# Performance work log

Measured on AMD Instinct MI355X. Metric: run time of the kernel, lower is better.

The kernel has to match this reference:

```python
import jax, jax.numpy as jnp
import numpy as np

EPS_DISC = 1e-9  # matches mamba_discretization denominator epsilon


def setup_inputs() -> dict:
    key = jax.random.key(0)
    ks = jax.random.split(key, 12)
    L, D, N, W = 2048, 1024, 16, 3
    s = 0.02  # small init scale to keep softplus/exp well-behaved
    u_seq = jax.random.normal(ks[0], (L, D), jnp.float32)
    # A_log = log(-A) with A = randn*0.1 - 1.0  -> log of a value near 1
    A_log = jnp.log(jnp.clip(1.0 - 0.1 * jax.random.normal(ks[1], (N,), jnp.float32), 0.5, 1.5))
    dt_w = jax.random.normal(ks[2], (D, D), jnp.float32) * s
    dt_b = jax.random.normal(ks[3], (D,), jnp.float32) * s
    B_w = jax.random.normal(ks[4], (N, D), jnp.float32) * s
    B_b = jax.random.normal(ks[5], (N,), jnp.float32) * s
    C_w = jax.random.normal(ks[6], (N, D), jnp.float32) * s
    C_b = jax.random.normal(ks[7], (N,), jnp.float32) * s
    D_w = jnp.ones((D,), jnp.float32)
    scale = jnp.ones((), jnp.float32)
    init_w = jax.random.normal(ks[8], (D * N, D * W), jnp.float32) * s
    init_b = jax.random.normal(ks[9], (D * N,), jnp.float32) * s
    return {"u_seq": u_seq, "A_log": A_log, "dt_w": dt_w, "dt_b": dt_b,
            "B_w": B_w, "B_b": B_b, "C_w": C_w, "C_b": C_b,
            "D_w": D_w, "scale": scale, "init_w": init_w, "init_b": init_b}


def reference(u_seq, A_log, dt_w, dt_b, B_w, B_b, C_w, C_b, D_w, scale, init_w, init_b):
    L, D = u_seq.shape
    N = A_log.shape[0]
    init_window = init_w.shape[1] // D
    # Initial state h0 = init_estimator(u[:W].flatten()).view(D, N)
    u_prefix = u_seq[:init_window].reshape(-1)
    h0 = (u_prefix @ init_w.T + init_b).reshape(D, N)
    # Input-dependent SSM parameters (all L timesteps at once)
    dt = jax.nn.softplus(u_seq @ dt_w.T + dt_b)           # [L, D]
    B = u_seq @ B_w.T + B_b                               # [L, N]
    C = u_seq @ C_w.T + C_b                               # [L, N]
    A = -jnp.exp(A_log)                                   # [N]
    dtA = dt[:, :, None] * A                              # [L, D, N]
    dA = jnp.exp(dtA)                                     # [L, D, N]
    dB = jnp.expm1(dtA) / (dtA + EPS_DISC) * B[:, None, :]  # ZOH discretization
    Bu = dB * u_seq[:, :, None]                           # [L, D, N]

    # Sequential selective-scan recurrence: h_t = dA_t * h_{t-1} + Bu_t
    def step(h, inp):
        dA_t, Bu_t = inp
        h = dA_t * h + Bu_t
        return h, h

    _, h_hist = jax.lax.scan(step, h0, (dA, Bu))          # [L, D, N]
    y_raw = jnp.einsum('ln,ldn->ld', C, h_hist) + D_w * u_seq
    return jax.nn.softplus(y_raw) * jnp.maximum(scale, 0.5)
```

## Files before the change

### kernel.cpp

```cpp
#include <hip/hip_runtime.h>
#include <hip/hip_bf16.h>

typedef __attribute__((ext_vector_type(8))) short short8v;
typedef __attribute__((ext_vector_type(4))) float f32x4;

#define L_SEQ 2048
#define D_DIM 1024
#define N_DIM 16
#define T_CHUNK 32
#define NCHUNK (L_SEQ / T_CHUNK)
#define EPS_DISC 1e-9f

__device__ __forceinline__ float softplusf(float x) {
    return (x > 15.f) ? x : __logf(1.f + __expf(x));
}

__device__ __forceinline__ unsigned short f2bf(float f) {
    unsigned int u = __float_as_uint(f);
    u += 0x7FFFu + ((u >> 16) & 1u);
    return (unsigned short)(u >> 16);
}
__device__ __forceinline__ unsigned int pack2(float a, float b) {
    return (unsigned int)f2bf(a) | ((unsigned int)f2bf(b) << 16);
}

__global__ __launch_bounds__(256) void fm_params(const float* __restrict__ u,
                                                 const float* __restrict__ dt_w,
                                                 const float* __restrict__ dt_b,
                                                 const float* __restrict__ B_w,
                                                 const float* __restrict__ B_b,
                                                 const float* __restrict__ C_w,
                                                 const float* __restrict__ C_b,
                                                 const float* __restrict__ init_w,
                                                 const float* __restrict__ init_b,
                                                 float* __restrict__ dt_out,
                                                 float* __restrict__ Bout,
                                                 float* __restrict__ Cout,
                                                 float* __restrict__ h0) {
    __shared__ unsigned int As[128 * 16];
    __shared__ unsigned int Bs[128 * 16];
    const int b = blockIdx.x;
    const int t = threadIdx.x;

    if (b < 128) {
        const int bm   = b & 15;
        const int bn   = b >> 4;
        const int row  = t >> 1;
        const int half = t & 1;
        const int swz  = (row >> 1) & 3;
        const int lane = t & 63;
        const int wid  = t >> 6;
        const int wm   = wid >> 1, wn = wid & 1;
        const int lrow = lane & 15, lq = lane >> 4;

        const float* uptr = u + (bm * 128 + row) * 1024 + half * 16;
        const float* wptr = dt_w + (bn * 128 + row) * 1024 + half * 16;

        f32x4 acc[4][4];
#pragma unroll
        for (int mi = 0; mi < 4; ++mi)
#pragma unroll
            for (int ni = 0; ni < 4; ++ni) acc[mi][ni] = (f32x4){0.f, 0.f, 0.f, 0.f};

        for (int k0 = 0; k0 < 1024; k0 += 32) {
            __syncthreads();
            {
                const float4* p = (const float4*)(uptr + k0);
                float4 a0 = p[0], a1 = p[1], a2 = p[2], a3 = p[3];
                uint4 c0 = make_uint4(pack2(a0.x, a0.y), pack2(a0.z, a0.w),
                                      pack2(a1.x, a1.y), pack2(a1.z, a1.w));
                uint4 c1 = make_uint4(pack2(a2.x, a2.y), pack2(a2.z, a2.w),
                                      pack2(a3.x, a3.y), pack2(a3.z, a3.w));
                const int kb0 = (half * 2) ^ swz, kb1 = (half * 2 + 1) ^ swz;
                *(uint4*)&As[row * 16 + kb0 * 4] = c0;
                *(uint4*)&As[row * 16 + kb1 * 4] = c1;

                const float4* q = (const float4*)(wptr + k0);
                float4 b0 = q[0], b1 = q[1], b2 = q[2], b3 = q[3];
                uint4 d0 = make_uint4(pack2(b0.x, b0.y), pack2(b0.z, b0.w),
                                      pack2(b1.x, b1.y), pack2(b1.z, b1.w));
                uint4 d1 = make_uint4(pack2(b2.x, b2.y), pack2(b2.z, b2.w),
                                      pack2(b3.x, b3.y), pack2(b3.z, b3.w));
                *(uint4*)&Bs[row * 16 + kb0 * 4] = d0;
                *(uint4*)&Bs[row * 16 + kb1 * 4] = d1;
            }
            __syncthreads();
            short8v af[4], bf[4];
#pragma unroll
            for (int mi = 0; mi < 4; ++mi) {
                const int ar = wm * 64 + mi * 16 + lrow;
                const int kb = lq ^ ((ar >> 1) & 3);
                af[mi] = *(const short8v*)&As[ar * 16 + kb * 4];
            }
#pragma unroll
            for (int ni = 0; ni < 4; ++ni) {
                const int br = wn * 64 + ni * 16 + lrow;
                const int kb = lq ^ ((br >> 1) & 3);
                bf[ni] = *(const short8v*)&Bs[br * 16 + kb * 4];
            }
#pragma unroll
            for (int mi = 0; mi < 4; ++mi)
#pragma unroll
                for (int ni = 0; ni < 4; ++ni)
                    acc[mi][ni] = __builtin_amdgcn_mfma_f32_16x16x32_bf16(af[mi], bf[ni], acc[mi][ni], 0, 0, 0);
        }

#pragma unroll
        for (int mi = 0; mi < 4; ++mi)
#pragma unroll
            for (int ni = 0; ni < 4; ++ni) {
                const int cg = bn * 128 + wn * 64 + ni * 16 + lrow;
                const float bv = dt_b[cg];
#pragma unroll
                for (int j = 0; j < 4; ++j) {
                    const int rg = bm * 128 + wm * 64 + mi * 16 + lq * 4 + j;
                    dt_out[rg * 1024 + cg] = softplusf(acc[mi][ni][j] + bv);
                }
            }
    } else if (b < 384) {
        const int tid = (b - 128) * 256 + t;
        const int l = tid >> 5;
        const int col = tid & 31;
        const float* wrow = (col < 16) ? (B_w + col * 1024) : (C_w + (col - 16) * 1024);
        const float4* w4 = (const float4*)wrow;
        const float4* u4 = (const float4*)(u + l * 1024);
        float acc = 0.f;
#pragma unroll 8
        for (int j = 0; j < 256; ++j) {
            float4 a = u4[j], bb = w4[j];
            acc += a.x * bb.x + a.y * bb.y + a.z * bb.z + a.w * bb.w;
        }
        if (col < 16) Bout[l * 16 + col] = acc + B_b[col];
        else          Cout[l * 16 + (col - 16)] = acc + C_b[col - 16];
    } else {
        const int lane = t & 63;
        const int row  = (b - 384) * 4 + (t >> 6);
        const float4* w4 = (const float4*)(init_w + row * 3072);
        const float4* u4 = (const float4*)u;
        float acc = 0.f;
#pragma unroll
        for (int s = 0; s < 12; ++s) {
            float4 a = w4[s * 64 + lane];
            float4 bb = u4[s * 64 + lane];
            acc += a.x * bb.x + a.y * bb.y + a.z * bb.z + a.w * bb.w;
        }
#pragma unroll
        for (int off = 32; off > 0; off >>= 1) acc += __shfl_down(acc, off);
        if (lane == 0) h0[row] = acc + init_b[row];
    }
}

__global__ __launch_bounds__(256) void fm_scan_phase1(const float* __restrict__ dt,
                                                      const float* __restrict__ Bm,
                                                      const float* __restrict__ u,
                                                      const float* __restrict__ A_log,
                                                      float* __restrict__ ap,
                                                      float* __restrict__ hl) {
    const int t = threadIdx.x;
    const int c = blockIdx.x >> 2;
    const int d = ((blockIdx.x & 3) << 8) | t;
    float An[16];
#pragma unroll
    for (int n = 0; n < 16; ++n) An[n] = -__expf(A_log[n]);
    float h[16], p[16];
#pragma unroll
    for (int n = 0; n < 16; ++n) { h[n] = 0.f; p[n] = 1.f; }

    const int l0 = c * T_CHUNK;
    for (int i = 0; i < T_CHUNK; ++i) {
        const int l = l0 + i;
        const float dtld = dt[l * D_DIM + d];
        const float uld  = u[l * D_DIM + d];
        const float4 b0 = *(const float4*)&Bm[l * 16 + 0];
        const float4 b1 = *(const float4*)&Bm[l * 16 + 4];
        const float4 b2 = *(const float4*)&Bm[l * 16 + 8];
        const float4 b3 = *(const float4*)&Bm[l * 16 + 12];
        auto body = [&](int n, float bn) {
            const float x = dtld * An[n];
            const float e = __expf(x);
            const float coef = (e - 1.f) * __builtin_amdgcn_rcpf(x + EPS_DISC);
            const float bu = coef * bn * uld;
            p[n] *= e;
            h[n] = fmaf(e, h[n], bu);
        };
        body(0, b0.x);  body(1, b0.y);  body(2, b0.z);  body(3, b0.w);
        body(4, b1.x);  body(5, b1.y);  body(6, b1.z);  body(7, b1.w);
        body(8, b2.x);  body(9, b2.y);  body(10, b2.z); body(11, b2.w);
        body(12, b3.x); body(13, b3.y); body(14, b3.z); body(15, b3.w);
    }
    const int base = c * (D_DIM * N_DIM) + d * 16;
    *(float4*)&ap[base + 0]  = make_float4(p[0], p[1], p[2], p[3]);
    *(float4*)&ap[base + 4]  = make_float4(p[4], p[5], p[6], p[7]);
    *(float4*)&ap[base + 8]  = make_float4(p[8], p[9], p[10], p[11]);
    *(float4*)&ap[base + 12] = make_float4(p[12], p[13], p[14], p[15]);
    *(float4*)&hl[base + 0]  = make_float4(h[0], h[1], h[2], h[3]);
    *(float4*)&hl[base + 4]  = make_float4(h[4], h[5], h[6], h[7]);
    *(float4*)&hl[base + 8]  = make_float4(h[8], h[9], h[10], h[11]);
    *(float4*)&hl[base + 12] = make_float4(h[12], h[13], h[14], h[15]);
}

__global__ __launch_bounds__(64) void fm_scan_phase2(const float* __restrict__ h0,
                                                     float* __restrict__ ap,
                                                     const float* __restrict__ hl) {
    const int tid = blockIdx.x * 64 + threadIdx.x;
    float h = h0[tid];
#pragma unroll 8
    for (int c = 0; c < NCHUNK; ++c) {
        const int idx = c * (D_DIM * N_DIM) + tid;
        const float a = ap[idx];
        const float b = hl[idx];
        ap[idx] = h;
        h = fmaf(a, h, b);
    }
}

__global__ __launch_bounds__(256) void fm_scan_phase3(const float* __restrict__ dt,
                                                      const float* __restrict__ Bm,
                                                      const float* __restrict__ Cm,
                                                      const float* __restrict__ u,
                                                      const float* __restrict__ A_log,
                                                      const float* __restrict__ hstart,
                                                      const float* __restrict__ D_w,
                                                      const float* __restrict__ scale,
                                                      float* __restrict__ out) {
    const int t = threadIdx.x;
    const int c = blockIdx.x >> 2;
    const int d = ((blockIdx.x & 3) << 8) | t;
    float An[16];
#pragma unroll
    for (int n = 0; n < 16; ++n) An[n] = -__expf(A_log[n]);
    float h[16];
    const int base = c * (D_DIM * N_DIM) + d * 16;
    {
        float4 h0v = *(const float4*)&hstart[base + 0];
        float4 h1v = *(const float4*)&hstart[base + 4];
        float4 h2v = *(const float4*)&hstart[base + 8];
        float4 h3v = *(const float4*)&hstart[base + 12];
        h[0] = h0v.x; h[1] = h0v.y; h[2] = h0v.z; h[3] = h0v.w;
        h[4] = h1v.x; h[5] = h1v.y; h[6] = h1v.z; h[7] = h1v.w;
        h[8] = h2v.x; h[9] = h2v.y; h[10] = h2v.z; h[11] = h2v.w;
        h[12] = h3v.x; h[13] = h3v.y; h[14] = h3v.z; h[15] = h3v.w;
    }
    const float scl = fmaxf(scale[0], 0.5f);
    const float dw = D_w[d];
    const int l0 = c * T_CHUNK;
    for (int i = 0; i < T_CHUNK; ++i) {
        const int l = l0 + i;
        const float dtld = dt[l * D_DIM + d];
        const float uld  = u[l * D_DIM + d];
        const float4 b0 = *(const float4*)&Bm[l * 16 + 0];
        const float4 b1 = *(const float4*)&Bm[l * 16 + 4];
        const float4 b2 = *(const float4*)&Bm[l * 16 + 8];
        const float4 b3 = *(const float4*)&Bm[l * 16 + 12];
        const float4 c0 = *(const float4*)&Cm[l * 16 + 0];
        const float4 c1 = *(const float4*)&Cm[l * 16 + 4];
        const float4 c2 = *(const float4*)&Cm[l * 16 + 8];
        const float4 c3 = *(const float4*)&Cm[l * 16 + 12];
        float y = 0.f;
        auto body = [&](int n, float bn, float cn) {
            const float x = dtld * An[n];
            const float e = __expf(x);
            const float coef = (e - 1.f) * __builtin_amdgcn_rcpf(x + EPS_DISC);
            const float bu = coef * bn * uld;
            h[n] = fmaf(e, h[n], bu);
            y = fmaf(cn, h[n], y);
        };
        body(0, b0.x, c0.x);   body(1, b0.y, c0.y);   body(2, b0.z, c0.z);   body(3, b0.w, c0.w);
        body(4, b1.x, c1.x);   body(5, b1.y, c1.y);   body(6, b1.z, c1.z);   body(7, b1.w, c1.w);
        body(8, b2.x, c2.x);   body(9, b2.y, c2.y);   body(10, b2.z, c2.z);  body(11, b2.w, c2.w);
        body(12, b3.x, c3.x);  body(13, b3.y, c3.y);  body(14, b3.z, c3.z);  body(15, b3.w, c3.w);
        y = fmaf(dw, uld, y);
        out[l * D_DIM + d] = softplusf(y) * scl;
    }
}

extern "C" void kernel_launch(void* const* d_in, const int* in_sizes, int n_in,
                              void* d_out, int out_size, void* d_ws, size_t ws_size,
                              hipStream_t stream) {
    const float* u      = (const float*)d_in[0];
    const float* A_log  = (const float*)d_in[1];
    const float* dt_w   = (const float*)d_in[2];
    const float* dt_b   = (const float*)d_in[3];
    const float* B_w    = (const float*)d_in[4];
    const float* B_b    = (const float*)d_in[5];
    const float* C_w    = (const float*)d_in[6];
    const float* C_b    = (const float*)d_in[7];
    const float* D_w    = (const float*)d_in[8];
    const float* scale  = (const float*)d_in[9];
    const float* init_w = (const float*)d_in[10];
    const float* init_b = (const float*)d_in[11];
    float* out = (float*)d_out;

    float* ws = (float*)d_ws;
    float* dt = ws;
    float* Bm = dt + 2097152;
    float* Cm = Bm + 32768;
    float* h0 = Cm + 32768;
    float* ap = h0 + 16384;
    float* hl = ap + 1048576;

    hipLaunchKernelGGL(fm_params, dim3(4480), dim3(256), 0, stream,
                       u, dt_w, dt_b, B_w, B_b, C_w, C_b, init_w, init_b,
                       dt, Bm, Cm, h0);
    hipLaunchKernelGGL(fm_scan_phase1, dim3(256), dim3(256), 0, stream, dt, Bm, u, A_log, ap, hl);
    hipLaunchKernelGGL(fm_scan_phase2, dim3(256), dim3(64), 0, stream, h0, ap, hl);
    hipLaunchKernelGGL(fm_scan_phase3, dim3(256), dim3(256), 0, stream, dt, Bm, Cm, u, A_log, ap, D_w, scale, out);
}
```

Before: 120.3 us.

## Fuse all phases into one cooperative persistent kernel with grid syncs

Merges the parameter GEMM, the chunk scan, the cross-chunk carry and the output pass into a single cooperative kernel that loops over tiles and separates phases with grid.sync. It also splits each channel's 16 states across two threads, doubling the thread count in the scan phases and combining the partial outputs with a shuffle. The aim is to remove launch gaps and tail effects between the four kernels and to use more of the GPU in the scan phases. In exchange, the GEMM phase now runs as a persistent loop with a grid limited by occupancy, plus the cost of the grid barriers, and the old four-kernel path is kept as a fallback.

```diff
diff --git a/kernel.cpp b/kernel.cpp
--- a/kernel.cpp
+++ b/kernel.cpp
@@ -1,5 +1,8 @@
 #include <hip/hip_runtime.h>
 #include <hip/hip_bf16.h>
+#include <hip/hip_cooperative_groups.h>
+
+namespace cg = cooperative_groups;
 
 typedef __attribute__((ext_vector_type(8))) short short8v;
 typedef __attribute__((ext_vector_type(4))) float f32x4;
@@ -24,27 +27,18 @@
     return (unsigned int)f2bf(a) | ((unsigned int)f2bf(b) << 16);
 }
 
-__global__ __launch_bounds__(256) void fm_params(const float* __restrict__ u,
-                                                 const float* __restrict__ dt_w,
-                                                 const float* __restrict__ dt_b,
-                                                 const float* __restrict__ B_w,
-                                                 const float* __restrict__ B_b,
-                                                 const float* __restrict__ C_w,
-                                                 const float* __restrict__ C_b,
-                                                 const float* __restrict__ init_w,
-                                                 const float* __restrict__ init_b,
-                                                 float* __restrict__ dt_out,
-                                                 float* __restrict__ Bout,
-                                                 float* __restrict__ Cout,
-                                                 float* __restrict__ h0) {
-    __shared__ unsigned int As[128 * 16];
-    __shared__ unsigned int Bs[128 * 16];
-    const int b = blockIdx.x;
+__device__ void phaseA_tile(int tile, unsigned int* As, unsigned int* Bs,
+                            const float* __restrict__ u,
+                            const float* __restrict__ dt_w, const float* __restrict__ dt_b,
+                            const float* __restrict__ B_w, const float* __restrict__ B_b,
+                            const float* __restrict__ C_w, const float* __restrict__ C_b,
+                            const float* __restrict__ init_w, const float* __restrict__ init_b,
+                            float* __restrict__ dt, float* __restrict__ Bm,
+                            float* __restrict__ Cm, float* __restrict__ h0) {
     const int t = threadIdx.x;
-
-    if (b < 128) {
-        const int bm   = b & 15;
-        const int bn   = b >> 4;
+    if (tile < 128) {
+        const int bm   = tile & 15;
+        const int bn   = tile >> 4;
         const int row  = t >> 1;
         const int half = t & 1;
         const int swz  = (row >> 1) & 3;
@@ -109,16 +103,17 @@
         for (int mi = 0; mi < 4; ++mi)
 #pragma unroll
             for (int ni = 0; ni < 4; ++ni) {
-                const int cg = bn * 128 + wn * 64 + ni * 16 + lrow;
-                const float bv = dt_b[cg];
+                const int cg_ = bn * 128 + wn * 64 + ni * 16 + lrow;
+                const float bv = dt_b[cg_];
 #pragma unroll
                 for (int j = 0; j < 4; ++j) {
                     const int rg = bm * 128 + wm * 64 + mi * 16 + lq * 4 + j;
-                    dt_out[rg * 1024 + cg] = softplusf(acc[mi][ni][j] + bv);
+                    dt[rg * 1024 + cg_] = softplusf(acc[mi][ni][j] + bv);
                 }
             }
-    } else if (b < 384) {
-        const int tid = (b - 128) * 256 + t;
+        __syncthreads();
+    } else if (tile < 384) {
+        const int tid = (tile - 128) * 256 + t;
         const int l = tid >> 5;
         const int col = tid & 31;
         const float* wrow = (col < 16) ? (B_w + col * 1024) : (C_w + (col - 16) * 1024);
@@ -130,11 +125,11 @@
             float4 a = u4[j], bb = w4[j];
             acc += a.x * bb.x + a.y * bb.y + a.z * bb.z + a.w * bb.w;
         }
-        if (col < 16) Bout[l * 16 + col] = acc + B_b[col];
-        else          Cout[l * 16 + (col - 16)] = acc + C_b[col - 16];
+        if (col < 16) Bm[l * 16 + col] = acc + B_b[col];
+        else          Cm[l * 16 + (col - 16)] = acc + C_b[col - 16];
     } else {
         const int lane = t & 63;
-        const int row  = (b - 384) * 4 + (t >> 6);
+        const int row  = (tile - 384) * 4 + (t >> 6);
         const float4* w4 = (const float4*)(init_w + row * 3072);
         const float4* u4 = (const float4*)u;
         float acc = 0.f;
@@ -150,31 +145,30 @@
     }
 }
 
-__global__ __launch_bounds__(256) void fm_scan_phase1(const float* __restrict__ dt,
-                                                      const float* __restrict__ Bm,
-                                                      const float* __restrict__ u,
-                                                      const float* __restrict__ A_log,
-                                                      float* __restrict__ ap,
-                                                      float* __restrict__ hl) {
-    const int t = threadIdx.x;
-    const int c = blockIdx.x >> 2;
-    const int d = ((blockIdx.x & 3) << 8) | t;
-    float An[16];
-#pragma unroll
-    for (int n = 0; n < 16; ++n) An[n] = -__expf(A_log[n]);
-    float h[16], p[16];
-#pragma unroll
-    for (int n = 0; n < 16; ++n) { h[n] = 0.f; p[n] = 1.f; }
+__device__ void phaseB_tile(int tile,
+                            const float* __restrict__ dt, const float* __restrict__ Bm,
+                            const float* __restrict__ u, const float* __restrict__ A_log,
+                            float* __restrict__ ap, float* __restrict__ hl) {
+    const int t    = threadIdx.x;
+    const int c    = tile >> 3;
+    const int dblk = tile & 7;
+    const int dd   = t >> 1;
+    const int nh   = t & 1;
+    const int d    = dblk * 128 + dd;
+    float An[8];
+#pragma unroll
+    for (int n = 0; n < 8; ++n) An[n] = -__expf(A_log[nh * 8 + n]);
+    float h[8], p[8];
+#pragma unroll
+    for (int n = 0; n < 8; ++n) { h[n] = 0.f; p[n] = 1.f; }
 
     const int l0 = c * T_CHUNK;
     for (int i = 0; i < T_CHUNK; ++i) {
         const int l = l0 + i;
         const float dtld = dt[l * D_DIM + d];
         const float uld  = u[l * D_DIM + d];
-        const float4 b0 = *(const float4*)&Bm[l * 16 + 0];
-        const float4 b1 = *(const float4*)&Bm[l * 16 + 4];
-        const float4 b2 = *(const float4*)&Bm[l * 16 + 8];
-        const float4 b3 = *(const float4*)&Bm[l * 16 + 12];
+        const float4 b0 = *(const float4*)&Bm[l * 16 + nh * 8];
+        const float4 b1 = *(const float4*)&Bm[l * 16 + nh * 8 + 4];
         auto body = [&](int n, float bn) {
             const float x = dtld * An[n];
             const float e = __expf(x);
@@ -183,63 +177,56 @@
             p[n] *= e;
             h[n] = fmaf(e, h[n], bu);
         };
-        body(0, b0.x);  body(1, b0.y);  body(2, b0.z);  body(3, b0.w);
-        body(4, b1.x);  body(5, b1.y);  body(6, b1.z);  body(7, b1.w);
-        body(8, b2.x);  body(9, b2.y);  body(10, b2.z); body(11, b2.w);
-        body(12, b3.x); body(13, b3.y); body(14, b3.z); body(15, b3.w);
-    }
-    const int base = c * (D_DIM * N_DIM) + d * 16;
-    *(float4*)&ap[base + 0]  = make_float4(p[0], p[1], p[2], p[3]);
-    *(float4*)&ap[base + 4]  = make_float4(p[4], p[5], p[6], p[7]);
-    *(float4*)&ap[base + 8]  = make_float4(p[8], p[9], p[10], p[11]);
-    *(float4*)&ap[base + 12] = make_float4(p[12], p[13], p[14], p[15]);
-    *(float4*)&hl[base + 0]  = make_float4(h[0], h[1], h[2], h[3]);
-    *(float4*)&hl[base + 4]  = make_float4(h[4], h[5], h[6], h[7]);
-    *(float4*)&hl[base + 8]  = make_float4(h[8], h[9], h[10], h[11]);
-    *(float4*)&hl[base + 12] = make_float4(h[12], h[13], h[14], h[15]);
-}
-
-__global__ __launch_bounds__(64) void fm_scan_phase2(const float* __restrict__ h0,
-                                                     float* __restrict__ ap,
-                                                     const float* __restrict__ hl) {
-    const int tid = blockIdx.x * 64 + threadIdx.x;
-    float h = h0[tid];
+        body(0, b0.x); body(1, b0.y); body(2, b0.z); body(3, b0.w);
+        body(4, b1.x); body(5, b1.y); body(6, b1.z); body(7, b1.w);
+    }
+    const int base = c * (D_DIM * N_DIM) + d * 16 + nh * 8;
+    *(float4*)&ap[base + 0] = make_float4(p[0], p[1], p[2], p[3]);
+    *(float4*)&ap[base + 4] = make_float4(p[4], p[5], p[6], p[7]);
+    *(float4*)&hl[base + 0] = make_float4(h[0], h[1], h[2], h[3]);
+    *(float4*)&hl[base + 4] = make_float4(h[4], h[5], h[6], h[7]);
+}
+
+__device__ void phaseC_group(int g,
+                             const float* __restrict__ h0,
+                             float* __restrict__ ap, const float* __restrict__ hl) {
+    const int t = threadIdx.x;
+    if (t < 64) {
+        const int ch = g * 64 + t;
+        float h = h0[ch];
 #pragma unroll 8
-    for (int c = 0; c < NCHUNK; ++c) {
-        const int idx = c * (D_DIM * N_DIM) + tid;
-        const float a = ap[idx];
-        const float b = hl[idx];
-        ap[idx] = h;
-        h = fmaf(a, h, b);
-    }
-}
-
-__global__ __launch_bounds__(256) void fm_scan_phase3(const float* __restrict__ dt,
-                                                      const float* __restrict__ Bm,
-                                                      const float* __restrict__ Cm,
-                                                      const float* __restrict__ u,
-                                                      const float* __restrict__ A_log,
-                                                      const float* __restrict__ hstart,
-                                                      const float* __restrict__ D_w,
-                                                      const float* __restrict__ scale,
-                                                      float* __restrict__ out) {
-    const int t = threadIdx.x;
-    const int c = blockIdx.x >> 2;
-    const int d = ((blockIdx.x & 3) << 8) | t;
-    float An[16];
-#pragma unroll
-    for (int n = 0; n < 16; ++n) An[n] = -__expf(A_log[n]);
-    float h[16];
-    const int base = c * (D_DIM * N_DIM) + d * 16;
+        for (int c = 0; c < NCHUNK; ++c) {
+            const int idx = c * (D_DIM * N_DIM) + ch;
+            const float a = ap[idx];
+            const float b = hl[idx];
+            ap[idx] = h;
+            h = fmaf(a, h, b);
+        }
+    }
+}
+
+__device__ void phaseD_tile(int tile,
+                            const float* __restrict__ dt, const float* __restrict__ Bm,
+                            const float* __restrict__ Cm, const float* __restrict__ u,
+                            const float* __restrict__ A_log, const float* __restrict__ hstart,
+                            const float* __restrict__ D_w, const float* __restrict__ scale,
+                            float* __restrict__ out) {
+    const int t    = threadIdx.x;
+    const int c    = tile >> 3;
+    const int dblk = tile & 7;
+    const int dd   = t >> 1;
+    const int nh   = t & 1;
+    const int d    = dblk * 128 + dd;
+    float An[8];
+#pragma unroll
+    for (int n = 0; n < 8; ++n) An[n] = -__expf(A_log[nh * 8 + n]);
+    float h[8];
+    const int base = c * (D_DIM * N_DIM) + d * 16 + nh * 8;
     {
         float4 h0v = *(const float4*)&hstart[base + 0];
         float4 h1v = *(const float4*)&hstart[base + 4];
-        float4 h2v = *(const float4*)&hstart[base + 8];
-        float4 h3v = *(const float4*)&hstart[base + 12];
         h[0] = h0v.x; h[1] = h0v.y; h[2] = h0v.z; h[3] = h0v.w;
         h[4] = h1v.x; h[5] = h1v.y; h[6] = h1v.z; h[7] = h1v.w;
-        h[8] = h2v.x; h[9] = h2v.y; h[10] = h2v.z; h[11] = h2v.w;
-        h[12] = h3v.x; h[13] = h3v.y; h[14] = h3v.z; h[15] = h3v.w;
     }
     const float scl = fmaxf(scale[0], 0.5f);
     const float dw = D_w[d];
@@ -248,14 +235,10 @@
         const int l = l0 + i;
         const float dtld = dt[l * D_DIM + d];
         const float uld  = u[l * D_DIM + d];
-        const float4 b0 = *(const float4*)&Bm[l * 16 + 0];
-        const float4 b1 = *(const float4*)&Bm[l * 16 + 4];
-        const float4 b2 = *(const float4*)&Bm[l * 16 + 8];
-        const float4 b3 = *(const float4*)&Bm[l * 16 + 12];
-        const float4 c0 = *(const float4*)&Cm[l * 16 + 0];
-        const float4 c1 = *(const float4*)&Cm[l * 16 + 4];
-        const float4 c2 = *(const float4*)&Cm[l * 16 + 8];
-        const float4 c3 = *(const float4*)&Cm[l * 16 + 12];
+        const float4 b0 = *(const float4*)&Bm[l * 16 + nh * 8];
+        const float4 b1 = *(const float4*)&Bm[l * 16 + nh * 8 + 4];
+        const float4 c0 = *(const float4*)&Cm[l * 16 + nh * 8];
+        const float4 c1 = *(const float4*)&Cm[l * 16 + nh * 8 + 4];
         float y = 0.f;
         auto body = [&](int n, float bn, float cn) {
             const float x = dtld * An[n];
@@ -265,13 +248,91 @@
             h[n] = fmaf(e, h[n], bu);
             y = fmaf(cn, h[n], y);
         };
-        body(0, b0.x, c0.x);   body(1, b0.y, c0.y);   body(2, b0.z, c0.z);   body(3, b0.w, c0.w);
-        body(4, b1.x, c1.x);   body(5, b1.y, c1.y);   body(6, b1.z, c1.z);   body(7, b1.w, c1.w);
-        body(8, b2.x, c2.x);   body(9, b2.y, c2.y);   body(10, b2.z, c2.z);  body(11, b2.w, c2.w);
-        body(12, b3.x, c3.x);  body(13, b3.y, c3.y);  body(14, b3.z, c3.z);  body(15, b3.w, c3.w);
-        y = fmaf(dw, uld, y);
-        out[l * D_DIM + d] = softplusf(y) * scl;
-    }
+        body(0, b0.x, c0.x); body(1, b0.y, c0.y); body(2, b0.z, c0.z); body(3, b0.w, c0.w);
+        body(4, b1.x, c1.x); body(5, b1.y, c1.y); body(6, b1.z, c1.z); body(7, b1.w, c1.w);
+        y += __shfl_xor(y, 1);
+        if (nh == 0) {
+            const float yv = fmaf(dw, uld, y);
+            out[l * D_DIM + d] = softplusf(yv) * scl;
+        }
+    }
+}
+
+__global__ __launch_bounds__(256, 2) void fm_mega(const float* __restrict__ u,
+                                                  const float* __restrict__ A_log,
+                                                  const float* __restrict__ dt_w,
+                                                  const float* __restrict__ dt_b,
+                                                  const float* __restrict__ B_w,
+                                                  const float* __restrict__ B_b,
+                                                  const float* __restrict__ C_w,
+                                                  const float* __restrict__ C_b,
+                                                  const float* __restrict__ D_w,
+                                                  const float* __restrict__ scale,
+                                                  const float* __restrict__ init_w,
+                                                  const float* __restrict__ init_b,
+                                                  float* __restrict__ dt,
+                                                  float* __restrict__ Bm,
+                                                  float* __restrict__ Cm,
+                                                  float* __restrict__ h0,
+                                                  float* __restrict__ ap,
+                                                  float* __restrict__ hl,
+                                                  float* __restrict__ out) {
+    cg::grid_group grid = cg::this_grid();
+    __shared__ unsigned int As[128 * 16];
+    __shared__ unsigned int Bs[128 * 16];
+    const int nb = gridDim.x;
+
+    for (int tile = blockIdx.x; tile < 4480; tile += nb)
+        phaseA_tile(tile, As, Bs, u, dt_w, dt_b, B_w, B_b, C_w, C_b, init_w, init_b, dt, Bm, Cm, h0);
+
+    __threadfence();
+    grid.sync();
+
+    for (int tile = blockIdx.x; tile < 512; tile += nb)
+        phaseB_tile(tile, dt, Bm, u, A_log, ap, hl);
+
+    __threadfence();
+    grid.sync();
+
+    for (int g = blockIdx.x; g < 256; g += nb)
+        phaseC_group(g, h0, ap, hl);
+
+    __threadfence();
+    grid.sync();
+
+    for (int tile = blockIdx.x; tile < 512; tile += nb)
+        phaseD_tile(tile, dt, Bm, Cm, u, A_log, ap, D_w, scale, out);
+}
+
+__global__ __launch_bounds__(256) void k_params(const float* __restrict__ u,
+                                                const float* __restrict__ dt_w, const float* __restrict__ dt_b,
+                                                const float* __restrict__ B_w, const float* __restrict__ B_b,
+                                                const float* __restrict__ C_w, const float* __restrict__ C_b,
+                                                const float* __restrict__ init_w, const float* __restrict__ init_b,
+                                                float* __restrict__ dt, float* __restrict__ Bm,
+                                                float* __restrict__ Cm, float* __restrict__ h0) {
+    __shared__ unsigned int As[128 * 16];
+    __shared__ unsigned int Bs[128 * 16];
+    phaseA_tile(blockIdx.x, As, Bs, u, dt_w, dt_b, B_w, B_b, C_w, C_b, init_w, init_b, dt, Bm, Cm, h0);
+}
+
+__global__ __launch_bounds__(256) void k_p1(const float* __restrict__ dt, const float* __restrict__ Bm,
+                                            const float* __restrict__ u, const float* __restrict__ A_log,
+                                            float* __restrict__ ap, float* __restrict__ hl) {
+    phaseB_tile(blockIdx.x, dt, Bm, u, A_log, ap, hl);
+}
+
+__global__ __launch_bounds__(64) void k_p2(const float* __restrict__ h0,
+                                           float* __restrict__ ap, const float* __restrict__ hl) {
+    phaseC_group(blockIdx.x, h0, ap, hl);
+}
+
+__global__ __launch_bounds__(256) void k_p3(const float* __restrict__ dt, const float* __restrict__ Bm,
+                                            const float* __restrict__ Cm, const float* __restrict__ u,
+                                            const float* __restrict__ A_log, const float* __restrict__ hstart,
+                                            const float* __restrict__ D_w, const float* __restrict__ scale,
+                                            float* __restrict__ out) {
+    phaseD_tile(blockIdx.x, dt, Bm, Cm, u, A_log, hstart, D_w, scale, out);
 }
 
 extern "C" void kernel_launch(void* const* d_in, const int* in_sizes, int n_in,
@@ -299,10 +360,28 @@
     float* ap = h0 + 16384;
     float* hl = ap + 1048576;
 
-    hipLaunchKernelGGL(fm_params, dim3(4480), dim3(256), 0, stream,
-                       u, dt_w, dt_b, B_w, B_b, C_w, C_b, init_w, init_b,
-                       dt, Bm, Cm, h0);
-    hipLaunchKernelGGL(fm_scan_phase1, dim3(256), dim3(256), 0, stream, dt, Bm, u, A_log, ap, hl);
-    hipLaunchKernelGGL(fm_scan_phase2, dim3(256), dim3(64), 0, stream, h0, ap, hl);
-    hipLaunchKernelGGL(fm_scan_phase3, dim3(256), dim3(256), 0, stream, dt, Bm, Cm, u, A_log, ap, D_w, scale, out);
-}
+    int coop = 0;
+    (void)hipDeviceGetAttribute(&coop, hipDeviceAttributeCooperativeLaunch, 0);
+    int maxBlk = 0;
+    (void)hipOccupancyMaxActiveBlocksPerMultiprocessor(&maxBlk, fm_mega, 256, 0);
+
+    hipError_t err = hipErrorUnknown;
+    if (coop && maxBlk >= 1) {
+        const int grid = (maxBlk >= 2) ? 512 : 256;
+        void* args[] = {
+            (void*)&u, (void*)&A_log, (void*)&dt_w, (void*)&dt_b,
+            (void*)&B_w, (void*)&B_b, (void*)&C_w, (void*)&C_b,
+            (void*)&D_w, (void*)&scale, (void*)&init_w, (void*)&init_b,
+            (void*)&dt, (void*)&Bm, (void*)&Cm, (void*)&h0,
+            (void*)&ap, (void*)&hl, (void*)&out,
+        };
+        err = hipLaunchCooperativeKernel((void*)fm_mega, dim3(grid), dim3(256), args, 0, stream);
+    }
+    if (err != hipSuccess) {
+        hipLaunchKernelGGL(k_params, dim3(4480), dim3(256), 0, stream,
+                           u, dt_w, dt_b, B_w, B_b, C_w, C_b, init_w, init_b, dt, Bm, Cm, h0);
+        hipLaunchKernelGGL(k_p1, dim3(512), dim3(256), 0, stream, dt, Bm, u, A_log, ap, hl);
+        hipLaunchKernelGGL(k_p2, dim3(256), dim3(64), 0, stream, h0, ap, hl);
+        hipLaunchKernelGGL(k_p3, dim3(512), dim3(256), 0, stream, dt, Bm, Cm, u, A_log, ap, D_w, scale, out);
+    }
+}
```

New measurement: 148.6 us. 1.24x slower.
